# Performance work log

Hardware: AMD Instinct MI355X
Metric: run time of the kernel (lower is better)

## Reference

```python
import jax, jax.numpy as jnp
import numpy as np

B, S, HID = 1, 4096, 1024
NH, HD = 16, 64            # heads, per-head dim
BS = 256                    # block size
PB = 256                    # position buckets (= max_relative_positions)
EPS = 1e-7


def make_log_bucket_position(rel, num_buckets, max_position):
    sign = jnp.sign(rel)
    max_exact = num_buckets // 2
    in_exact = (rel < max_exact) & (rel > -max_exact)
    abs_pos = jnp.where(in_exact, max_exact - 1, jnp.abs(rel))
    x = jnp.log((max_position - 1) / max_exact)
    xx = jnp.log(abs_pos / max_exact) / x
    log_pos = jnp.ceil(xx * (max_exact - 1)) + max_exact
    return jnp.where(abs_pos <= max_exact, rel, (log_pos * sign).astype(jnp.int32)).astype(jnp.int32)


def split_into_blocks(x, block_size, axis):
    # [..., S, ...] -> [..., S//bs, bs, ...]; S assumed divisible by bs
    shp = x.shape
    new = shp[:axis] + (shp[axis] // block_size, block_size) + shp[axis + 1:]
    return x.reshape(new)


def concat_3_blocks(x, block_axis, seq_axis, pad_value=0):
    # pad one zero block on each side of the block axis, then concat
    # [prev, cur, next] along the within-block seq axis.
    pad = [(0, 0)] * x.ndim
    pad[block_axis] = (1, 1)
    xp = jnp.pad(x, pad, constant_values=pad_value)
    nb = x.shape[block_axis]
    slices = [jax.lax.dynamic_slice_in_dim(xp, i, nb, block_axis) for i in range(3)]
    return jnp.concatenate(slices, axis=seq_axis)


def layer_norm(x, scale, bias):
    mu = jnp.mean(x, axis=-1, keepdims=True)
    var = jnp.mean(jnp.square(x - mu), axis=-1, keepdims=True)
    return (x - mu) * jax.lax.rsqrt(var + EPS) * scale + bias


def setup_inputs() -> dict:
    key = jax.random.key(0)
    ks = jax.random.split(key, 8)
    d = {
        'hidden_states': jax.random.normal(ks[0], (B, S, HID), jnp.float32) * 0.02,
        'rel_pos_embeddings': jax.random.normal(ks[1], (S, HID), jnp.float32) * 0.02,
        'Wq': jax.random.normal(ks[2], (HID, HID), jnp.float32) * 0.01,
        'bq': jnp.zeros((HID,), jnp.float32),
        'Wk': jax.random.normal(ks[3], (HID, HID), jnp.float32) * 0.01,
        'bk': jnp.zeros((HID,), jnp.float32),
        'Wv': jax.random.normal(ks[4], (HID, HID), jnp.float32) * 0.01,
        'bv': jnp.zeros((HID,), jnp.float32),
        'Wo': jax.random.normal(ks[5], (HID, HID), jnp.float32) * 0.01,
        'bo': jnp.zeros((HID,), jnp.float32),
        'ln_scale': jnp.ones((HID,), jnp.float32),
        'ln_bias': jnp.zeros((HID,), jnp.float32),
    }
    return d


def reference(hidden_states, rel_pos_embeddings, Wq, bq, Wk, bk, Wv, bv, Wo, bo, ln_scale, ln_bias):
    b, s, hid = hidden_states.shape

    def heads(x):
        return x.reshape(x.shape[:-1] + (NH, HD))

    # content projections -> [B, nb, bs, h, d]
    q = split_into_blocks(heads(hidden_states @ Wq + bq), BS, axis=1)
    k = split_into_blocks(heads(hidden_states @ Wk + bk), BS, axis=1)
    v = split_into_blocks(heads(hidden_states @ Wv + bv), BS, axis=1)
    k3 = concat_3_blocks(k, block_axis=1, seq_axis=2)   # [B, nb, 3bs, h, d]
    v3 = concat_3_blocks(v, block_axis=1, seq_axis=2)

    c2c = jnp.einsum('bnqhd,bnkhd->bnhqk', q, k3)

    # position projections, stacked over batch (size-1 batch dim broadcasts in einsum)
    pos_q = split_into_blocks(heads(rel_pos_embeddings @ Wq + bq)[None], BS, axis=1)  # [1, nb, bs, h, d]
    pos_k = split_into_blocks(heads(rel_pos_embeddings @ Wk + bk)[None], BS, axis=1)
    pos_k3 = concat_3_blocks(pos_k, block_axis=1, seq_axis=2)                          # [1, nb, 3bs, h, d]

    rel = jnp.arange(BS, dtype=jnp.int32)[:, None] - jnp.arange(3 * BS, dtype=jnp.int32)[None, :]
    rel = make_log_bucket_position(rel, PB, PB)
    idx = jnp.clip(rel + PB, 0, 2 * PB - 1)            # [bs, 3bs]

    c2p = jnp.einsum('bnqhd,bnkhd->bnhqk', q, pos_k3)  # [B, nb, h, bs, 3bs]
    # faithful to the source: axis-less jnp.take gathers from the FLATTENED
    # score tensor -> [bs, 3bs] bias broadcast over (batch, block, head)
    c2p_bias = jnp.take(c2p, idx)

    p2c = jnp.einsum('bnqhd,bnkhd->bnhqk', pos_q, k3)
    p2c_bias = jnp.take(p2c, idx)

    scale = jnp.sqrt(jnp.asarray(HD * 3, hidden_states.dtype))
    attn = (c2c + c2p_bias + p2c_bias) / scale
    probs = jax.nn.softmax(attn, axis=-1)

    ctx = jnp.einsum('bnhqk,bnkhd->bnqhd', probs, v3)  # [B, nb, bs, h, d]
    ctx = ctx.reshape(b, s, hid)
    out = ctx @ Wo + bo
    return layer_norm(out + hidden_states, ln_scale, ln_bias)
```

## Files before the change

kernel.cpp:

```cpp
#include <hip/hip_runtime.h>
#include <stdint.h>

typedef unsigned short u16;
typedef __bf16 bf16_t;
typedef bf16_t v8bf __attribute__((ext_vector_type(8)));
typedef float v4f __attribute__((ext_vector_type(4)));

#define SEQ   4096
#define HIDN  1024
#define NHEAD 16
#define HDIM  64
#define BLK   256
#define NBLK  16

#define GLOAD_LDS16(g, l) __builtin_amdgcn_global_load_lds( \
  (const __attribute__((address_space(1))) unsigned*)(g), \
  (__attribute__((address_space(3))) unsigned*)(l), 16, 0, 0)

__device__ __forceinline__ u16 f2bf(float f){
  union { float f; unsigned u; } v; v.f = f;
  unsigned r = (v.u + 0x7fffu + ((v.u >> 16) & 1u)) >> 16;
  return (u16)r;
}
__device__ __forceinline__ float bf2f(u16 h){
  union { unsigned u; float f; } v; v.u = ((unsigned)h) << 16;
  return v.f;
}

__global__ __launch_bounds__(256) void k_prep(const float* __restrict__ hidden, u16* __restrict__ hb,
    const float* __restrict__ Wq, const float* __restrict__ Wk,
    const float* __restrict__ Wv, const float* __restrict__ Wo, u16* __restrict__ Wt,
    const float* __restrict__ bq, const float* __restrict__ bk, const float* __restrict__ bv,
    float* __restrict__ bcat,
    const float* __restrict__ rpe, float* __restrict__ posk, float* __restrict__ posq0)
{
  __shared__ float t[32][33];
  __shared__ float red[4][64];
  int b = blockIdx.x, tid = threadIdx.x;
  if (b < 4096){
    int w = b >> 10, tile = b & 1023;
    int k0 = (tile & 31) * 32, n0 = (tile >> 5) * 32;
    const float* W = (w == 0) ? Wq : (w == 1) ? Wk : (w == 2) ? Wv : Wo;
    u16* outp = Wt + (size_t)w * 1024 * 1024;
    int x = tid & 31, y = tid >> 5;
    #pragma unroll
    for (int yy = 0; yy < 32; yy += 8) t[y + yy][x] = W[(size_t)(k0 + y + yy) * 1024 + n0 + x];
    __syncthreads();
    #pragma unroll
    for (int yy = 0; yy < 32; yy += 8) outp[(size_t)(n0 + y + yy) * 1024 + k0 + x] = f2bf(t[x][y + yy]);
  } else if (b < 4608){
    int base = (b - 4096) * 8192;
    #pragma unroll
    for (int j = 0; j < 8; j++){
      int i = base + j * 1024 + tid * 4;
      float4 f = *(const float4*)&hidden[i];
      unsigned u0 = (unsigned)f2bf(f.x) | ((unsigned)f2bf(f.y) << 16);
      unsigned u1 = (unsigned)f2bf(f.z) | ((unsigned)f2bf(f.w) << 16);
      uint2 p; p.x = u0; p.y = u1;
      *(uint2*)&hb[i] = p;
    }
  } else if (b == 4608){
    #pragma unroll
    for (int j = 0; j < 12; j++){
      int i = j * 256 + tid;
      const float* src = i < 1024 ? bq : (i < 2048 ? bk : bv);
      bcat[i] = src[i & 1023];
    }
  } else {
    int pb = b - 4609;
    int d = tid & 63, part = tid >> 6;
    const float* W  = (pb < 256) ? Wk : Wq;
    const float* rv = (pb < 256) ? &rpe[(size_t)pb * 1024] : rpe;
    float s = 0.f;
    for (int k = part * 256; k < part * 256 + 256; k++) s += rv[k] * W[(size_t)k * 1024 + d];
    red[part][d] = s;
    __syncthreads();
    if (part == 0){
      s = red[0][d] + red[1][d] + red[2][d] + red[3][d];
      if (pb < 256) posk[pb * 64 + d] = s + bk[d];
      else          posq0[d] = s + bq[d];
    }
  }
}

__global__ __launch_bounds__(256) void k_gemm_qkv(const u16* __restrict__ A, const u16* __restrict__ Bt,
                                                  const float* __restrict__ bias,
                                                  u16* __restrict__ qk, u16* __restrict__ Vt)
{
  __shared__ alignas(16) u16 As[128 * 32];
  __shared__ alignas(16) u16 Bs[128 * 32];
  int tid = threadIdx.x, lane = tid & 63, wid = tid >> 6;
  int wr = wid >> 1, wc = wid & 1;
  int m0 = blockIdx.y * 128, n0 = blockIdx.x * 128;
  const int K = 1024;

  v4f acc[4][4];
  #pragma unroll
  for (int m = 0; m < 4; m++)
    #pragma unroll
    for (int n = 0; n < 4; n++) acc[m][n] = (v4f){0.f, 0.f, 0.f, 0.f};

  int r = lane & 15, g = lane >> 4;
  int ob0 = wid * 2048;

  for (int kt = 0; kt < K; kt += 32){
    #pragma unroll
    for (int t = 0; t < 2; ++t){
      int ob = ob0 + t * 1024;
      int o  = ob + lane * 16;
      int row = o >> 6, col = (o & 63) >> 1;
      GLOAD_LDS16(&A [(size_t)(m0 + row) * K + kt + col], As + (ob >> 1));
      GLOAD_LDS16(&Bt[(size_t)(n0 + row) * K + kt + col], Bs + (ob >> 1));
    }
    __syncthreads();
    v8bf a[4], bb[4];
    #pragma unroll
    for (int m = 0; m < 4; m++) a[m] = *(const v8bf*)&As[(wr * 64 + m * 16 + r) * 32 + g * 8];
    #pragma unroll
    for (int n = 0; n < 4; n++) bb[n] = *(const v8bf*)&Bs[(wc * 64 + n * 16 + r) * 32 + g * 8];
    #pragma unroll
    for (int m = 0; m < 4; m++)
      #pragma unroll
      for (int n = 0; n < 4; n++)
        acc[m][n] = __builtin_amdgcn_mfma_f32_16x16x32_bf16(a[m], bb[n], acc[m][n], 0, 0, 0);
    __syncthreads();
  }

  #pragma unroll
  for (int m = 0; m < 4; m++)
    #pragma unroll
    for (int n = 0; n < 4; n++){
      int col = n0 + wc * 64 + n * 16 + r;
      float bv = bias[col];
      #pragma unroll
      for (int i = 0; i < 4; i++){
        int row = m0 + wr * 64 + m * 16 + g * 4 + i;
        u16 h = f2bf(acc[m][n][i] + bv);
        if (col < 2048) qk[(size_t)row * 2048 + col] = h;
        else            Vt[(size_t)(col - 2048) * 4096 + row] = h;
      }
    }
}

__global__ __launch_bounds__(256) void k_gemm_out(const u16* __restrict__ A, const u16* __restrict__ Bt,
                                                  const float* __restrict__ bias,
                                                  const float* __restrict__ resid, float* __restrict__ Cout)
{
  __shared__ alignas(16) u16 As[128 * 32];
  __shared__ alignas(16) u16 Bs[128 * 32];
  int tid = threadIdx.x, lane = tid & 63, wid = tid >> 6;
  int wr = wid >> 1, wc = wid & 1;
  int m0 = blockIdx.y * 128, n0 = blockIdx.x * 128;
  const int K = 1024;

  v4f acc[4][4];
  #pragma unroll
  for (int m = 0; m < 4; m++)
    #pragma unroll
    for (int n = 0; n < 4; n++) acc[m][n] = (v4f){0.f, 0.f, 0.f, 0.f};

  int r = lane & 15, g = lane >> 4;
  int ob0 = wid * 2048;

  for (int kt = 0; kt < K; kt += 32){
    #pragma unroll
    for (int t = 0; t < 2; ++t){
      int ob = ob0 + t * 1024;
      int o  = ob + lane * 16;
      int row = o >> 6, col = (o & 63) >> 1;
      GLOAD_LDS16(&A [(size_t)(m0 + row) * K + kt + col], As + (ob >> 1));
      GLOAD_LDS16(&Bt[(size_t)(n0 + row) * K + kt + col], Bs + (ob >> 1));
    }
    __syncthreads();
    v8bf a[4], bb[4];
    #pragma unroll
    for (int m = 0; m < 4; m++) a[m] = *(const v8bf*)&As[(wr * 64 + m * 16 + r) * 32 + g * 8];
    #pragma unroll
    for (int n = 0; n < 4; n++) bb[n] = *(const v8bf*)&Bs[(wc * 64 + n * 16 + r) * 32 + g * 8];
    #pragma unroll
    for (int m = 0; m < 4; m++)
      #pragma unroll
      for (int n = 0; n < 4; n++)
        acc[m][n] = __builtin_amdgcn_mfma_f32_16x16x32_bf16(a[m], bb[n], acc[m][n], 0, 0, 0);
    __syncthreads();
  }

  #pragma unroll
  for (int m = 0; m < 4; m++)
    #pragma unroll
    for (int n = 0; n < 4; n++){
      int col = n0 + wc * 64 + n * 16 + r;
      float bv = bias[col];
      #pragma unroll
      for (int i = 0; i < 4; i++){
        int row = m0 + wr * 64 + m * 16 + g * 4 + i;
        Cout[(size_t)row * 1024 + col] = acc[m][n][i] + bv + resid[(size_t)row * 1024 + col];
      }
    }
}

__global__ __launch_bounds__(256) void k_bias(const u16* __restrict__ qk,
                                              const float* __restrict__ posk, const float* __restrict__ posq0,
                                              float* __restrict__ biasd)
{
  __shared__ float brow[512];
  int tid = threadIdx.x;
  brow[tid] = 0.f;
  {
    int u = tid;
    float c2p = 0.f, p2c = 0.f;
    for (int d = 0; d < 64; d++){
      c2p += bf2f(qk[d]) * posk[u * 64 + d];
      p2c += posq0[d] * bf2f(qk[(size_t)u * 2048 + 1024 + d]);
    }
    brow[256 + u] = c2p + p2c;
  }
  __syncthreads();
  #pragma unroll
  for (int j = 0; j < 4; j++){
    int t = tid + j * 256;
    int rel = t - 767;
    int bucket;
    bool in_exact = (rel < 128) && (rel > -128);
    int abs_pos = in_exact ? 127 : (rel < 0 ? -rel : rel);
    if (abs_pos <= 128) bucket = rel;
    else {
      float xx = logf((float)abs_pos * (1.0f / 128.0f)) / logf(255.0f / 128.0f);
      float lp = ceilf(xx * 127.0f) + 128.0f;
      int sgn = (rel > 0) ? 1 : ((rel < 0) ? -1 : 0);
      bucket = (int)lp * sgn;
    }
    int idx = bucket + 256;
    idx = idx < 0 ? 0 : (idx > 511 ? 511 : idx);
    biasd[t] = brow[idx];
  }
}

__global__ __launch_bounds__(256) void k_attn(const u16* __restrict__ qk, const u16* __restrict__ Vt,
                                              const float* __restrict__ biasd, u16* __restrict__ ctxg)
{
  __shared__ alignas(16) u16 Qs[16 * 64];
  __shared__ alignas(16) u16 KVs[8192];
  __shared__ alignas(16) u16 Ss[16 * 776];
  __shared__ float bias_s[1024];
  __shared__ float wmax[64];
  __shared__ float invsum[16];

  int b = blockIdx.x;
  int qt = b & 15, h = (b >> 4) & 15, n = b >> 8;
  int tid = threadIdx.x, lane = tid & 63, w = tid >> 6;
  int q0 = n * 256 + qt * 16;
  int qb0 = qt * 16;
  int g0 = (n - 1) * 256;
  const float inv_scale = 0.07216878364870323f;

  int r = lane & 15, g = lane >> 4;

  if (w < 2){
    int o = w * 1024 + lane * 16;
    int row = o >> 7, p = (o >> 4) & 7;
    GLOAD_LDS16(&qk[(size_t)(q0 + row) * 2048 + h * 64 + ((p ^ (row & 7)) * 8)],
                ((u16*)Qs) + w * 512);
  }
  *(float4*)&bias_s[tid * 4] = *(const float4*)&biasd[tid * 4];

  float m4[4];
  #pragma unroll
  for (int i = 0; i < 4; i++) m4[i] = -3.0e38f;

  for (int c = 0; c < 6; ++c){
    int cb = g0 + c * 128;
    bool oob = (cb < 0) || (cb >= SEQ);
    if (!oob){
      #pragma unroll
      for (int t = 0; t < 4; ++t){
        int o = (w * 4 + t) * 1024 + lane * 16;
        int row = o >> 7, p = (o >> 4) & 7;
        GLOAD_LDS16(&qk[(size_t)(cb + row) * 2048 + 1024 + h * 64 + ((p ^ (row & 7)) * 8)],
                    ((u16*)KVs) + (w * 4 + t) * 512);
      }
    }
    __syncthreads();
    v4f sacc[2];
    sacc[0] = (v4f){0.f,0.f,0.f,0.f};
    sacc[1] = (v4f){0.f,0.f,0.f,0.f};
    if (!oob){
      #pragma unroll
      for (int ks = 0; ks < 2; ++ks){
        v8bf a = *(const v8bf*)&Qs[r * 64 + ((4 * ks + g) ^ (r & 7)) * 8];
        #pragma unroll
        for (int nn = 0; nn < 2; nn++){
          int kr = w * 32 + nn * 16 + r;
          v8bf bb = *(const v8bf*)&KVs[kr * 64 + ((4 * ks + g) ^ (kr & 7)) * 8];
          sacc[nn] = __builtin_amdgcn_mfma_f32_16x16x32_bf16(a, bb, sacc[nn], 0, 0, 0);
        }
      }
    }
    #pragma unroll
    for (int nn = 0; nn < 2; nn++){
      int kcol = c * 128 + w * 32 + nn * 16 + r;
      int scol = kcol ^ (g << 4);
      #pragma unroll
      for (int i = 0; i < 4; i++){
        int qrow = g * 4 + i;
        float sc = (sacc[nn][i] + bias_s[qb0 + qrow - kcol + 767]) * inv_scale;
        m4[i] = fmaxf(m4[i], sc);
        Ss[qrow * 776 + scol] = f2bf(sc);
      }
    }
    __syncthreads();
  }

  #pragma unroll
  for (int i = 0; i < 4; i++){
    m4[i] = fmaxf(m4[i], __shfl_xor(m4[i], 1));
    m4[i] = fmaxf(m4[i], __shfl_xor(m4[i], 2));
    m4[i] = fmaxf(m4[i], __shfl_xor(m4[i], 4));
    m4[i] = fmaxf(m4[i], __shfl_xor(m4[i], 8));
  }
  if (r == 0){
    #pragma unroll
    for (int i = 0; i < 4; i++) wmax[w * 16 + g * 4 + i] = m4[i];
  }
  __syncthreads();

  {
    int row = tid >> 4, sub = tid & 15;
    float mx = fmaxf(fmaxf(wmax[row], wmax[16 + row]), fmaxf(wmax[32 + row], wmax[48 + row]));
    u16* srow = &Ss[row * 776 + sub * 48];
    float sm = 0.f;
    #pragma unroll
    for (int ii = 0; ii < 6; ii++){
      uint4 pk = *(const uint4*)&srow[ii * 8];
      unsigned* wd = (unsigned*)&pk;
      #pragma unroll
      for (int j = 0; j < 4; j++){
        float e0 = __expf(bf2f((u16)(wd[j] & 0xffff)) - mx);
        float e1 = __expf(bf2f((u16)(wd[j] >> 16)) - mx);
        sm += e0 + e1;
        wd[j] = (unsigned)f2bf(e0) | ((unsigned)f2bf(e1) << 16);
      }
      *(uint4*)&srow[ii * 8] = pk;
    }
    sm += __shfl_xor(sm, 1);
    sm += __shfl_xor(sm, 2);
    sm += __shfl_xor(sm, 4);
    sm += __shfl_xor(sm, 8);
    if (sub == 0) invsum[row] = 1.0f / sm;
  }
  __syncthreads();

  v4f pacc = (v4f){0.f,0.f,0.f,0.f};
  int key = (r >> 2) & 3;
  for (int c = 0; c < 6; ++c){
    int cb = g0 + c * 128;
    bool oob = (cb < 0) || (cb >= SEQ);
    if (!oob){
      #pragma unroll
      for (int t = 0; t < 4; ++t){
        int o = (w * 4 + t) * 1024 + lane * 16;
        int d = o >> 8, p = (o >> 4) & 15;
        GLOAD_LDS16(&Vt[(size_t)(h * 64 + d) * 4096 + cb + ((p ^ (d & 7)) * 8)],
                    ((u16*)KVs) + (w * 4 + t) * 512);
      }
    }
    __syncthreads();
    if (!oob){
      int d = w * 16 + r;
      #pragma unroll
      for (int ks = 0; ks < 4; ++ks){
        int col = (c * 128 + ks * 32 + g * 8) ^ (key << 4);
        v8bf a  = *(const v8bf*)&Ss[r * 776 + col];
        v8bf bb = *(const v8bf*)&KVs[d * 128 + ((4 * ks + g) ^ (r & 7)) * 8];
        pacc = __builtin_amdgcn_mfma_f32_16x16x32_bf16(a, bb, pacc, 0, 0, 0);
      }
    }
    __syncthreads();
  }
  {
    int d = w * 16 + r;
    #pragma unroll
    for (int i = 0; i < 4; i++){
      int qrow = g * 4 + i;
      ctxg[(size_t)(q0 + qrow) * 1024 + h * 64 + d] = f2bf(pacc[i] * invsum[qrow]);
    }
  }
}

__global__ __launch_bounds__(256) void k_ln(float* __restrict__ out,
                                            const float* __restrict__ gamma, const float* __restrict__ beta)
{
  __shared__ float red[8];
  int row = blockIdx.x, tid = threadIdx.x;
  int lane = tid & 63, wid = tid >> 6;
  size_t base = (size_t)row * 1024 + tid * 4;
  float4 xv = *(const float4*)&out[base];
  float v0 = xv.x, v1 = xv.y, v2 = xv.z, v3 = xv.w;
  float s = v0 + v1 + v2 + v3;
  float q = v0 * v0 + v1 * v1 + v2 * v2 + v3 * v3;
  #pragma unroll
  for (int o = 32; o; o >>= 1){ s += __shfl_down(s, o); q += __shfl_down(q, o); }
  if (lane == 0){ red[wid] = s; red[4 + wid] = q; }
  __syncthreads();
  float ts = red[0] + red[1] + red[2] + red[3];
  float tq = red[4] + red[5] + red[6] + red[7];
  float mu = ts * (1.0f / 1024.0f);
  float var = tq * (1.0f / 1024.0f) - mu * mu;
  float rstd = rsqrtf(var + 1e-7f);
  int c = tid * 4;
  out[base + 0] = (v0 - mu) * rstd * gamma[c + 0] + beta[c + 0];
  out[base + 1] = (v1 - mu) * rstd * gamma[c + 1] + beta[c + 1];
  out[base + 2] = (v2 - mu) * rstd * gamma[c + 2] + beta[c + 2];
  out[base + 3] = (v3 - mu) * rstd * gamma[c + 3] + beta[c + 3];
}

extern "C" void kernel_launch(void* const* d_in, const int* in_sizes, int n_in,
                              void* d_out, int out_size, void* d_ws, size_t ws_size,
                              hipStream_t stream)
{
  const float* hidden = (const float*)d_in[0];
  const float* rpe    = (const float*)d_in[1];
  const float* Wq = (const float*)d_in[2];
  const float* bq = (const float*)d_in[3];
  const float* Wk = (const float*)d_in[4];
  const float* bk = (const float*)d_in[5];
  const float* Wv = (const float*)d_in[6];
  const float* bv = (const float*)d_in[7];
  const float* Wo = (const float*)d_in[8];
  const float* bo = (const float*)d_in[9];
  const float* lns = (const float*)d_in[10];
  const float* lnb = (const float*)d_in[11];
  float* out = (float*)d_out;

  char* ws = (char*)d_ws;
  size_t off = 0;
  auto alloc = [&](size_t bytes){ void* p = ws + off; off += (bytes + 255) & ~(size_t)255; return p; };
  u16* hb      = (u16*)alloc((size_t)SEQ * HIDN * 2);
  u16* Wt      = (u16*)alloc((size_t)4 * HIDN * HIDN * 2);
  u16* qk      = (u16*)alloc((size_t)SEQ * 2048 * 2);
  u16* Vt      = (u16*)alloc((size_t)HIDN * SEQ * 2);
  u16* ctxb    = (u16*)alloc((size_t)SEQ * HIDN * 2);
  float* bcat  = (float*)alloc(3072 * 4);
  float* poskf = (float*)alloc(256 * 64 * 4);
  float* posq0 = (float*)alloc(64 * 4);
  float* biasd = (float*)alloc(1024 * 4);
  (void)ws_size; (void)in_sizes; (void)n_in; (void)out_size;

  k_prep<<<4866, 256, 0, stream>>>(hidden, hb, Wq, Wk, Wv, Wo, Wt,
                                   bq, bk, bv, bcat, rpe, poskf, posq0);

  k_gemm_qkv<<<dim3(24, 32), 256, 0, stream>>>(hb, Wt, bcat, qk, Vt);

  k_bias<<<1, 256, 0, stream>>>(qk, poskf, posq0, biasd);

  k_attn<<<NBLK * NHEAD * 16, 256, 0, stream>>>(qk, Vt, biasd, ctxb);

  k_gemm_out<<<dim3(8, 32), 256, 0, stream>>>(ctxb, Wt + (size_t)3 * HIDN * HIDN, bo, hidden, out);

  k_ln<<<SEQ, 256, 0, stream>>>(out, lns, lnb);
}
```

Baseline: 174.4 us.

## Keep attention scores in registers for softmax and parallelize bias-row kernel

The attention kernel now keeps all 48 score values per thread in registers instead of writing bf16 scores to LDS and re-reading them for the exp pass. Softmax is done in the base-2 domain with exp2f, and row sums are reduced through shuffles plus a small LDS array. This removes a round of LDS traffic and a bf16 rounding of the pre-exp scores, at the cost of higher register pressure. Separately, the single-block bias kernel is split into an 8-block dot-product kernel that uses shuffle reduction and a small gather kernel, adding one extra launch.

```diff
diff --git a/kernel.cpp b/kernel.cpp
--- a/kernel.cpp
+++ b/kernel.cpp
@@ -199,41 +199,44 @@
     }
 }
 
-__global__ __launch_bounds__(256) void k_bias(const u16* __restrict__ qk,
+__global__ __launch_bounds__(256) void k_brow(const u16* __restrict__ qk,
                                               const float* __restrict__ posk, const float* __restrict__ posq0,
-                                              float* __restrict__ biasd)
-{
-  __shared__ float brow[512];
-  int tid = threadIdx.x;
-  brow[tid] = 0.f;
-  {
-    int u = tid;
-    float c2p = 0.f, p2c = 0.f;
-    for (int d = 0; d < 64; d++){
-      c2p += bf2f(qk[d]) * posk[u * 64 + d];
-      p2c += posq0[d] * bf2f(qk[(size_t)u * 2048 + 1024 + d]);
-    }
-    brow[256 + u] = c2p + p2c;
-  }
-  __syncthreads();
-  #pragma unroll
-  for (int j = 0; j < 4; j++){
-    int t = tid + j * 256;
-    int rel = t - 767;
-    int bucket;
-    bool in_exact = (rel < 128) && (rel > -128);
-    int abs_pos = in_exact ? 127 : (rel < 0 ? -rel : rel);
-    if (abs_pos <= 128) bucket = rel;
-    else {
-      float xx = logf((float)abs_pos * (1.0f / 128.0f)) / logf(255.0f / 128.0f);
-      float lp = ceilf(xx * 127.0f) + 128.0f;
-      int sgn = (rel > 0) ? 1 : ((rel < 0) ? -1 : 0);
-      bucket = (int)lp * sgn;
-    }
-    int idx = bucket + 256;
-    idx = idx < 0 ? 0 : (idx > 511 ? 511 : idx);
-    biasd[t] = brow[idx];
-  }
+                                              float* __restrict__ brow)
+{
+  int b = blockIdx.x, tid = threadIdx.x;
+  if (tid < 32) brow[b * 32 + tid] = 0.f;
+  int u = b * 32 + (tid >> 3), sub = tid & 7;
+  float c2p = 0.f, p2c = 0.f;
+  #pragma unroll
+  for (int j = 0; j < 8; j++){
+    int d = sub * 8 + j;
+    c2p += bf2f(qk[d]) * posk[u * 64 + d];
+    p2c += posq0[d] * bf2f(qk[(size_t)u * 2048 + 1024 + d]);
+  }
+  float v = c2p + p2c;
+  v += __shfl_xor(v, 1);
+  v += __shfl_xor(v, 2);
+  v += __shfl_xor(v, 4);
+  if (sub == 0) brow[256 + u] = v;
+}
+
+__global__ void k_biasd(const float* __restrict__ brow, float* __restrict__ biasd)
+{
+  int t = blockIdx.x * blockDim.x + threadIdx.x;
+  int rel = t - 767;
+  int bucket;
+  bool in_exact = (rel < 128) && (rel > -128);
+  int abs_pos = in_exact ? 127 : (rel < 0 ? -rel : rel);
+  if (abs_pos <= 128) bucket = rel;
+  else {
+    float xx = logf((float)abs_pos * (1.0f / 128.0f)) / logf(255.0f / 128.0f);
+    float lp = ceilf(xx * 127.0f) + 128.0f;
+    int sgn = (rel > 0) ? 1 : ((rel < 0) ? -1 : 0);
+    bucket = (int)lp * sgn;
+  }
+  int idx = bucket + 256;
+  idx = idx < 0 ? 0 : (idx > 511 ? 511 : idx);
+  biasd[t] = brow[idx];
 }
 
 __global__ __launch_bounds__(256) void k_attn(const u16* __restrict__ qk, const u16* __restrict__ Vt,
@@ -243,8 +246,7 @@
   __shared__ alignas(16) u16 KVs[8192];
   __shared__ alignas(16) u16 Ss[16 * 776];
   __shared__ float bias_s[1024];
-  __shared__ float wmax[64];
-  __shared__ float invsum[16];
+  __shared__ float wred[64];
 
   int b = blockIdx.x;
   int qt = b & 15, h = (b >> 4) & 15, n = b >> 8;
@@ -252,7 +254,7 @@
   int q0 = n * 256 + qt * 16;
   int qb0 = qt * 16;
   int g0 = (n - 1) * 256;
-  const float inv_scale = 0.07216878364870323f;
+  const float c1 = 0.07216878364870323f * 1.4426950408889634f;
 
   int r = lane & 15, g = lane >> 4;
 
@@ -267,7 +269,9 @@
   float m4[4];
   #pragma unroll
   for (int i = 0; i < 4; i++) m4[i] = -3.0e38f;
-
+  v4f sc[6][2];
+
+  #pragma unroll
   for (int c = 0; c < 6; ++c){
     int cb = g0 + c * 128;
     bool oob = (cb < 0) || (cb >= SEQ);
@@ -299,13 +303,11 @@
     #pragma unroll
     for (int nn = 0; nn < 2; nn++){
       int kcol = c * 128 + w * 32 + nn * 16 + r;
-      int scol = kcol ^ (g << 4);
       #pragma unroll
       for (int i = 0; i < 4; i++){
-        int qrow = g * 4 + i;
-        float sc = (sacc[nn][i] + bias_s[qb0 + qrow - kcol + 767]) * inv_scale;
-        m4[i] = fmaxf(m4[i], sc);
-        Ss[qrow * 776 + scol] = f2bf(sc);
+        float s = (sacc[nn][i] + bias_s[qb0 + g * 4 + i - kcol + 767]) * c1;
+        m4[i] = fmaxf(m4[i], s);
+        sc[c][nn] [i] = s;
       }
     }
     __syncthreads();
@@ -320,35 +322,50 @@
   }
   if (r == 0){
     #pragma unroll
-    for (int i = 0; i < 4; i++) wmax[w * 16 + g * 4 + i] = m4[i];
+    for (int i = 0; i < 4; i++) wred[w * 16 + g * 4 + i] = m4[i];
   }
   __syncthreads();
-
-  {
-    int row = tid >> 4, sub = tid & 15;
-    float mx = fmaxf(fmaxf(wmax[row], wmax[16 + row]), fmaxf(wmax[32 + row], wmax[48 + row]));
-    u16* srow = &Ss[row * 776 + sub * 48];
-    float sm = 0.f;
-    #pragma unroll
-    for (int ii = 0; ii < 6; ii++){
-      uint4 pk = *(const uint4*)&srow[ii * 8];
-      unsigned* wd = (unsigned*)&pk;
-      #pragma unroll
-      for (int j = 0; j < 4; j++){
-        float e0 = __expf(bf2f((u16)(wd[j] & 0xffff)) - mx);
-        float e1 = __expf(bf2f((u16)(wd[j] >> 16)) - mx);
-        sm += e0 + e1;
-        wd[j] = (unsigned)f2bf(e0) | ((unsigned)f2bf(e1) << 16);
-      }
-      *(uint4*)&srow[ii * 8] = pk;
-    }
-    sm += __shfl_xor(sm, 1);
-    sm += __shfl_xor(sm, 2);
-    sm += __shfl_xor(sm, 4);
-    sm += __shfl_xor(sm, 8);
-    if (sub == 0) invsum[row] = 1.0f / sm;
+  float mrow[4];
+  #pragma unroll
+  for (int i = 0; i < 4; i++){
+    int row = g * 4 + i;
+    mrow[i] = fmaxf(fmaxf(wred[row], wred[16 + row]), fmaxf(wred[32 + row], wred[48 + row]));
+  }
+
+  float s4[4] = {0.f, 0.f, 0.f, 0.f};
+  #pragma unroll
+  for (int c = 0; c < 6; ++c){
+    #pragma unroll
+    for (int nn = 0; nn < 2; nn++){
+      int kcol = c * 128 + w * 32 + nn * 16 + r;
+      int scol = kcol ^ (g << 4);
+      #pragma unroll
+      for (int i = 0; i < 4; i++){
+        float p = exp2f(sc[c][nn][i] - mrow[i]);
+        s4[i] += p;
+        Ss[(g * 4 + i) * 776 + scol] = f2bf(p);
+      }
+    }
+  }
+  #pragma unroll
+  for (int i = 0; i < 4; i++){
+    s4[i] += __shfl_xor(s4[i], 1);
+    s4[i] += __shfl_xor(s4[i], 2);
+    s4[i] += __shfl_xor(s4[i], 4);
+    s4[i] += __shfl_xor(s4[i], 8);
   }
   __syncthreads();
+  if (r == 0){
+    #pragma unroll
+    for (int i = 0; i < 4; i++) wred[w * 16 + g * 4 + i] = s4[i];
+  }
+  __syncthreads();
+  float inv4[4];
+  #pragma unroll
+  for (int i = 0; i < 4; i++){
+    int row = g * 4 + i;
+    inv4[i] = 1.0f / (wred[row] + wred[16 + row] + wred[32 + row] + wred[48 + row]);
+  }
 
   v4f pacc = (v4f){0.f,0.f,0.f,0.f};
   int key = (r >> 2) & 3;
@@ -382,7 +399,7 @@
     #pragma unroll
     for (int i = 0; i < 4; i++){
       int qrow = g * 4 + i;
-      ctxg[(size_t)(q0 + qrow) * 1024 + h * 64 + d] = f2bf(pacc[i] * invsum[qrow]);
+      ctxg[(size_t)(q0 + qrow) * 1024 + h * 64 + d] = f2bf(pacc[i] * inv4[i]);
     }
   }
 }
@@ -443,6 +460,7 @@
   float* bcat  = (float*)alloc(3072 * 4);
   float* poskf = (float*)alloc(256 * 64 * 4);
   float* posq0 = (float*)alloc(64 * 4);
+  float* brow  = (float*)alloc(512 * 4);
   float* biasd = (float*)alloc(1024 * 4);
   (void)ws_size; (void)in_sizes; (void)n_in; (void)out_size;
 
@@ -451,7 +469,8 @@
 
   k_gemm_qkv<<<dim3(24, 32), 256, 0, stream>>>(hb, Wt, bcat, qk, Vt);
 
-  k_bias<<<1, 256, 0, stream>>>(qk, poskf, posq0, biasd);
+  k_brow<<<8, 256, 0, stream>>>(qk, poskf, posq0, brow);
+  k_biasd<<<4, 256, 0, stream>>>(brow, biasd);
 
   k_attn<<<NBLK * NHEAD * 16, 256, 0, stream>>>(qk, Vt, biasd, ctxb);
 
```

After: 172.6 us. No clear change (-1.0%).
